# Kernel tuning notes

Hardware: AMD Instinct MI355X
Metric: run time of the kernel (lower is better)

## Reference

```python
import jax, jax.numpy as jnp
import numpy as np

C, H_HEADS, L_LEV, M_PTS = 256, 4, 3, 4
TAU0 = 1.0


def _ln(x, g, b, eps=1e-5):
    mu = x.mean(-1, keepdims=True)
    var = ((x - mu) ** 2).mean(-1, keepdims=True)
    return (x - mu) * jax.lax.rsqrt(var + eps) * g + b


def _grid_sample(v, grid):
    """Bilinear grid_sample, padding_mode='zeros', align_corners=True.
    v: [B,C,Hin,Win], grid: [B,N,2] (x,y) in [-1,1] -> [B,N,C]"""
    B, Cc, Hin, Win = v.shape
    x = (grid[..., 0] + 1.0) * 0.5 * (Win - 1)
    y = (grid[..., 1] + 1.0) * 0.5 * (Hin - 1)
    x0 = jnp.floor(x); y0 = jnp.floor(y)
    wx1 = x - x0; wy1 = y - y0
    x0i = x0.astype(jnp.int32); y0i = y0.astype(jnp.int32)
    vflat = v.reshape(B, Cc, Hin * Win).transpose(0, 2, 1)  # [B,HW,C]

    def tap(yi, xi, w):
        valid = ((xi >= 0) & (xi < Win) & (yi >= 0) & (yi < Hin)).astype(v.dtype)
        idx = jnp.clip(yi, 0, Hin - 1) * Win + jnp.clip(xi, 0, Win - 1)  # [B,N]
        g = jax.vmap(lambda vf, i: vf[i])(vflat, idx)  # [B,N,C]
        return g * (w * valid)[..., None]

    return (tap(y0i, x0i, (1 - wy1) * (1 - wx1))
            + tap(y0i, x0i + 1, (1 - wy1) * wx1)
            + tap(y0i + 1, x0i, wy1 * (1 - wx1))
            + tap(y0i + 1, x0i + 1, wy1 * wx1))


def setup_inputs() -> dict:
    key = jax.random.key(0)
    ks = jax.random.split(key, 32)
    B, Hq, Wq = 2, 64, 64
    cins = [256, 512, 1024]
    d = {
        'S':  jax.random.normal(ks[0], (B, C, Hq, Wq), jnp.float32),
        'f0': jax.random.normal(ks[1], (B, cins[0], 64, 64), jnp.float32),
        'f1': jax.random.normal(ks[2], (B, cins[1], 32, 32), jnp.float32),
        'f2': jax.random.normal(ks[3], (B, cins[2], 16, 16), jnp.float32),
        'sim': jax.random.uniform(ks[4], (B, 1, Hq, Wq), jnp.float32),
        # 1x1 conv value projections per level
        'vw0': jax.random.normal(ks[5], (C, cins[0]), jnp.float32) * 0.02,
        'vb0': jnp.zeros((C,), jnp.float32),
        'vw1': jax.random.normal(ks[6], (C, cins[1]), jnp.float32) * 0.02,
        'vb1': jnp.zeros((C,), jnp.float32),
        'vw2': jax.random.normal(ks[7], (C, cins[2]), jnp.float32) * 0.02,
        'vb2': jnp.zeros((C,), jnp.float32),
        'q_w': jax.random.normal(ks[8], (C, C), jnp.float32) * 0.02,
        'q_b': jnp.zeros((C,), jnp.float32),
        # offset/weight predictors (non-zero so sampling is nontrivial)
        'off_w': jax.random.normal(ks[9], (H_HEADS * L_LEV * M_PTS * 2, C), jnp.float32) * 0.01,
        'off_b': jnp.zeros((H_HEADS * L_LEV * M_PTS * 2,), jnp.float32),
        'wgt_w': jax.random.normal(ks[10], (H_HEADS * L_LEV * M_PTS, C), jnp.float32) * 0.02,
        'wgt_b': jnp.zeros((H_HEADS * L_LEV * M_PTS,), jnp.float32),
        'out_w': jax.random.normal(ks[11], (C, H_HEADS * C), jnp.float32) * 0.02,
        'out_b': jnp.zeros((C,), jnp.float32),
        'lnq_g': jnp.ones((C,), jnp.float32), 'lnq_b': jnp.zeros((C,), jnp.float32),
        'lno_g': jnp.ones((C,), jnp.float32), 'lno_b': jnp.zeros((C,), jnp.float32),
        'fc1_w': jax.random.normal(ks[12], (4 * C, C), jnp.float32) * 0.02,
        'fc1_b': jnp.zeros((4 * C,), jnp.float32),
        'fc2_w': jax.random.normal(ks[13], (C, 4 * C), jnp.float32) * 0.02,
        'fc2_b': jnp.zeros((C,), jnp.float32),
    }
    return d


def reference(S, f0, f1, f2, sim, vw0, vb0, vw1, vb1, vw2, vb2, q_w, q_b,
              off_w, off_b, wgt_w, wgt_b, out_w, out_b,
              lnq_g, lnq_b, lno_g, lno_b, fc1_w, fc1_b, fc2_w, fc2_b):
    B, Cc, Hq, Wq = S.shape
    Nq = Hq * Wq
    S_seq = S.reshape(B, Cc, Nq).transpose(0, 2, 1)  # [B,Nq,C]
    Q = _ln(S_seq @ q_w.T + q_b, lnq_g, lnq_b)

    # reference points in [0,1], (x,y)
    ys = jnp.linspace(0.5 / Hq, 1 - 0.5 / Hq, Hq)
    xs = jnp.linspace(0.5 / Wq, 1 - 0.5 / Wq, Wq)
    yy, xx = jnp.meshgrid(ys, xs, indexing='ij')
    ref = jnp.stack([xx, yy], axis=-1).reshape(1, Nq, 2)

    feats = [(f0, vw0, vb0), (f1, vw1, vb1), (f2, vw2, vb2)]
    V = [jnp.einsum('bchw,oc->bohw', f, w) + b[None, :, None, None] for f, w, b in feats]

    off = (Q @ off_w.T + off_b).reshape(B, Nq, H_HEADS, L_LEV, M_PTS, 2)
    wts = (Q @ wgt_w.T + wgt_b).reshape(B, Nq, H_HEADS, L_LEV, M_PTS)

    sim2 = sim[:, 0].reshape(B, Nq, 1)
    tau = TAU0 / (sim2 + 0.001)
    wts = wts / tau.reshape(B, Nq, 1, 1, 1)
    wts = jax.nn.softmax(wts.reshape(B, Nq, H_HEADS, L_LEV * M_PTS), axis=-1)
    wts = wts.reshape(B, Nq, H_HEADS, L_LEV, M_PTS)

    acc = jnp.zeros((B, Nq, H_HEADS, Cc), S.dtype)
    for l in range(L_LEV):
        g01 = ref.reshape(1, Nq, 1, 1, 2) + off[:, :, :, l]  # [B,Nq,H,M,2]
        g = jnp.clip(jnp.tanh(g01 * 2.0 - 1.0), -1.0, 1.0)
        samp = _grid_sample(V[l], g.reshape(B, Nq * H_HEADS * M_PTS, 2))
        samp = samp.reshape(B, Nq, H_HEADS, M_PTS, Cc)
        acc = acc + jnp.einsum('bqhmc,bqhm->bqhc', samp, wts[:, :, :, l])

    Y = acc.reshape(B, Nq, H_HEADS * Cc) @ out_w.T + out_b
    Z = _ln(S_seq + Y, lno_g, lno_b)
    h = jax.nn.gelu(Z @ fc1_w.T + fc1_b, approximate=False)
    Z = Z + (h @ fc2_w.T + fc2_b)
    return Z.transpose(0, 2, 1).reshape(B, Cc, Hq, Wq)
```

## Files before the change

kernel.cpp:

```cpp
#include <hip/hip_runtime.h>
#include <hip/hip_bf16.h>
#include <math.h>

#define NQ 4096
#define CC 256

typedef __attribute__((ext_vector_type(8))) short bfrag;
typedef __attribute__((ext_vector_type(4))) float ffrag;

__device__ inline unsigned short f2bf(float x) {
  __hip_bfloat16 h = __float2bfloat16(x);
  return *reinterpret_cast<unsigned short*>(&h);
}

__device__ inline float bf2f(unsigned short u) {
  return __uint_as_float(((unsigned)u) << 16);
}

__device__ inline void gload16(const void* g, void* l) {
  __builtin_amdgcn_global_load_lds(
      (const __attribute__((address_space(1))) void*)g,
      (__attribute__((address_space(3))) void*)l, 16, 0, 0);
}

__device__ void tr64(const float* __restrict__ src,
                     unsigned short* __restrict__ dstb, int Cin, int P,
                     int p0, int c0, int b, float (*t)[73]) {
  int tid = threadIdx.x;
  int rx = tid & 15, ry = tid >> 4;
  const float* Sb = src + (size_t)b * Cin * P + p0 + rx * 4;
  #pragma unroll
  for (int i = 0; i < 4; i++) {
    int r = ry + i * 16;
    float4 v = *(const float4*)(Sb + (size_t)(c0 + r) * P);
    t[r][rx * 4 + 0] = v.x; t[r][rx * 4 + 1] = v.y;
    t[r][rx * 4 + 2] = v.z; t[r][rx * 4 + 3] = v.w;
  }
  __syncthreads();
  size_t ob = (size_t)b * P * Cin;
  #pragma unroll
  for (int i = 0; i < 4; i++) {
    int pr = ry + i * 16;
    float x0 = t[rx * 4 + 0][pr], x1 = t[rx * 4 + 1][pr];
    float x2 = t[rx * 4 + 2][pr], x3 = t[rx * 4 + 3][pr];
    size_t idx = ob + (size_t)(p0 + pr) * Cin + c0 + rx * 4;
    ushort4 u4;
    u4.x = f2bf(x0); u4.y = f2bf(x1); u4.z = f2bf(x2); u4.w = f2bf(x3);
    *(ushort4*)(dstb + idx) = u4;
  }
}

__global__ __launch_bounds__(256)
void prep_all_k(const float* S, const float* f0, const float* f1, const float* f2,
                const float* q_w, const float* off_w, const float* wgt_w,
                const float* vw0, const float* vw1, const float* vw2,
                const float* out_w, const float* fc1_w, const float* fc2_w,
                const float* off_b, const float* wgt_b,
                unsigned short* Sbf,
                unsigned short* Xf0, unsigned short* Xf1, unsigned short* Xf2,
                unsigned short* q_wb, unsigned short* owb,
                unsigned short* vw0b, unsigned short* vw1b, unsigned short* vw2b,
                unsigned short* out_wb, unsigned short* fc1_wb,
                unsigned short* fc2_wb, float* bias144) {
  __shared__ float t[64][73];
  int bid = blockIdx.x;
  if (bid < 512) {
    int l = bid;
    tr64(S, Sbf, 256, 4096, (l & 63) * 64, ((l >> 6) & 3) * 64, l >> 8, t);
  } else if (bid < 1024) {
    int l = bid - 512;
    tr64(f0, Xf0, 256, 4096, (l & 63) * 64, ((l >> 6) & 3) * 64, l >> 8, t);
  } else if (bid < 1280) {
    int l = bid - 1024;
    tr64(f1, Xf1, 512, 1024, (l & 15) * 64, ((l >> 4) & 7) * 64, l >> 7, t);
  } else if (bid < 1408) {
    int l = bid - 1280;
    tr64(f2, Xf2, 1024, 256, (l & 3) * 64, ((l >> 2) & 15) * 64, l >> 6, t);
  } else if (bid < 2688) {
    int i4 = (bid - 1408) * 256 + threadIdx.x;
    const float* src; unsigned short* dst;
    if (i4 < 16384)       { src = q_w;   dst = q_wb; }
    else if (i4 < 32768)  { i4 -= 16384;  src = vw0;   dst = vw0b; }
    else if (i4 < 65536)  { i4 -= 32768;  src = vw1;   dst = vw1b; }
    else if (i4 < 131072) { i4 -= 65536;  src = vw2;   dst = vw2b; }
    else if (i4 < 196608) { i4 -= 131072; src = out_w; dst = out_wb; }
    else if (i4 < 262144) { i4 -= 196608; src = fc1_w; dst = fc1_wb; }
    else                  { i4 -= 262144; src = fc2_w; dst = fc2_wb; }
    float4 v = ((const float4*)src)[i4];
    ushort4 u; u.x = f2bf(v.x); u.y = f2bf(v.y); u.z = f2bf(v.z); u.w = f2bf(v.w);
    ((ushort4*)dst)[i4] = u;
  } else {
    int e = (bid - 2688) * 256 + threadIdx.x;
    float v = (e < 24576) ? off_w[e] : (e < 36864 ? wgt_w[e - 24576] : 0.f);
    owb[e] = f2bf(v);
    if (e < 96) bias144[e] = off_b[e];
    else if (e < 144) bias144[e] = wgt_b[e - 96];
  }
}

template<int BM, int BN, int WM, int WN, int EPI>
__device__ __forceinline__ void gemm_body(
    const unsigned short* __restrict__ A, const unsigned short* __restrict__ B,
    const float* __restrict__ bias, float* __restrict__ outf,
    unsigned short* __restrict__ outb, int N, int Kloop, int lda, int ldb,
    int ldo, const unsigned short* __restrict__ Zres, float* __restrict__ outT,
    int m0, int n0, unsigned short* As, unsigned short* Bs) {
  constexpr int MI = BM / (WM * 16), NI = BN / (WN * 16);
  constexpr int TA = BM / 8, TB = BN / 8;
  constexpr int LBM = (BM == 32) ? 5 : (BM == 64) ? 6 : 7;
  constexpr int LBN = (BN == 64) ? 6 : (BN == 128) ? 7 : 8;
  int tid = threadIdx.x, wave = tid >> 6, lane = tid & 63;
  int quad = lane >> 4, l16 = lane & 15;
  int wm = wave / WN, wn = wave % WN;
  const int mbase = wm * (BM / WM), nbase = wn * (BN / WN);

  ffrag acc[MI][NI];
  #pragma unroll
  for (int i = 0; i < MI; i++)
    #pragma unroll
    for (int j = 0; j < NI; j++) acc[i][j] = (ffrag)0.f;

  for (int k0 = 0; k0 < Kloop; k0 += 64) {
    __syncthreads();
    for (int t = wave; t < TA + TB; t += 4) {
      if (t < TA) {
        int s = t * 64 + lane;
        int kc = s >> LBM, r = s & (BM - 1);
        gload16(A + (size_t)(m0 + r) * lda + k0 + kc * 8, (char*)As + t * 1024);
      } else {
        int s = (t - TA) * 64 + lane;
        int kc = s >> LBN, r = s & (BN - 1);
        gload16(B + (size_t)(n0 + r) * ldb + k0 + kc * 8, (char*)Bs + (t - TA) * 1024);
      }
    }
    __syncthreads();
    #pragma unroll
    for (int ks = 0; ks < 2; ks++) {
      bfrag af[MI], bf[NI];
      #pragma unroll
      for (int mi = 0; mi < MI; mi++)
        af[mi] = *(const bfrag*)(As + ((((ks * 4 + quad) << LBM) + mbase + mi * 16 + l16) << 3));
      #pragma unroll
      for (int ni = 0; ni < NI; ni++)
        bf[ni] = *(const bfrag*)(Bs + ((((ks * 4 + quad) << LBN) + nbase + ni * 16 + l16) << 3));
      #pragma unroll
      for (int mi = 0; mi < MI; mi++)
        #pragma unroll
        for (int ni = 0; ni < NI; ni++)
          acc[mi][ni] = __builtin_amdgcn_mfma_f32_16x16x32_bf16(
              af[mi], bf[ni], acc[mi][ni], 0, 0, 0);
    }
  }

  if (EPI == 2) {
    #pragma unroll
    for (int mi = 0; mi < MI; mi++) {
      int mrow = m0 + mbase + mi * 16 + quad * 4;
      int bb = mrow >> 12, q0 = mrow & (NQ - 1);
      #pragma unroll
      for (int ni = 0; ni < NI; ni++) {
        int n = n0 + nbase + ni * 16 + l16;
        float bv = bias[n];
        float4 v;
        v.x = acc[mi][ni][0] + bv + bf2f(Zres[(size_t)(mrow + 0) * CC + n]);
        v.y = acc[mi][ni][1] + bv + bf2f(Zres[(size_t)(mrow + 1) * CC + n]);
        v.z = acc[mi][ni][2] + bv + bf2f(Zres[(size_t)(mrow + 2) * CC + n]);
        v.w = acc[mi][ni][3] + bv + bf2f(Zres[(size_t)(mrow + 3) * CC + n]);
        *(float4*)(outT + ((size_t)(bb * CC + n)) * NQ + q0) = v;
      }
    }
  } else {
    #pragma unroll
    for (int mi = 0; mi < MI; mi++) {
      int mrow = m0 + mbase + mi * 16 + quad * 4;
      #pragma unroll
      for (int ni = 0; ni < NI; ni++) {
        int n = n0 + nbase + ni * 16 + l16;
        if (n < N) {
          float bv = (EPI == 4) ? 0.f : bias[n];
          #pragma unroll
          for (int r = 0; r < 4; r++) {
            float v = acc[mi][ni][r] + bv;
            if (EPI == 1) {
              v = 0.5f * v * (1.f + erff(v * 0.70710678118654752f));
              outb[(size_t)(mrow + r) * ldo + n] = f2bf(v);
            } else if (EPI == 3) {
              outb[(size_t)(mrow + r) * ldo + n] = f2bf(v);
            } else {
              outf[(size_t)(mrow + r) * ldo + n] = v;
            }
          }
        }
      }
    }
  }
}

__device__ __forceinline__ void gemm_ln_q(
    const unsigned short* __restrict__ A, const unsigned short* __restrict__ B,
    const float* __restrict__ bias, unsigned short* __restrict__ outb,
    const float* __restrict__ g, const float* __restrict__ be,
    int m0, char* sm) {
  unsigned short* As = (unsigned short*)sm;
  unsigned short* Bs = (unsigned short*)(sm + 4096);
  float* L = (float*)sm;
  const int K = 256;

  int tid = threadIdx.x, wave = tid >> 6, lane = tid & 63;
  int quad = lane >> 4, l16 = lane & 15;

  ffrag acc[2][4];
  #pragma unroll
  for (int i = 0; i < 2; i++)
    #pragma unroll
    for (int j = 0; j < 4; j++) acc[i][j] = (ffrag)0.f;

  for (int k0 = 0; k0 < K; k0 += 64) {
    __syncthreads();
    for (int t = wave; t < 36; t += 4) {
      if (t < 4) {
        int s = t * 64 + lane;
        int kc = s >> 5, r = s & 31;
        gload16(A + (size_t)(m0 + r) * K + k0 + kc * 8, sm + t * 1024);
      } else {
        int s = (t - 4) * 64 + lane;
        int kc = s >> 8, r = s & 255;
        gload16(B + (size_t)r * K + k0 + kc * 8, sm + 4096 + (t - 4) * 1024);
      }
    }
    __syncthreads();
    #pragma unroll
    for (int ks = 0; ks < 2; ks++) {
      bfrag af[2], bf[4];
      #pragma unroll
      for (int mi = 0; mi < 2; mi++)
        af[mi] = *(const bfrag*)(As + ((((ks * 4 + quad) << 5) + mi * 16 + l16) << 3));
      #pragma unroll
      for (int ni = 0; ni < 4; ni++)
        bf[ni] = *(const bfrag*)(Bs + ((((ks * 4 + quad) << 8) + wave * 64 + ni * 16 + l16) << 3));
      #pragma unroll
      for (int mi = 0; mi < 2; mi++)
        #pragma unroll
        for (int ni = 0; ni < 4; ni++)
          acc[mi][ni] = __builtin_amdgcn_mfma_f32_16x16x32_bf16(
              af[mi], bf[ni], acc[mi][ni], 0, 0, 0);
    }
  }
  __syncthreads();

  #pragma unroll
  for (int mi = 0; mi < 2; mi++) {
    int row = mi * 16 + quad * 4;
    #pragma unroll
    for (int ni = 0; ni < 4; ni++) {
      int col = wave * 64 + ni * 16 + l16;
      float bv = bias[col];
      #pragma unroll
      for (int r = 0; r < 4; r++)
        L[(row + r) * 264 + col] = acc[mi][ni][r] + bv;
    }
  }
  __syncthreads();

  int row = tid >> 3, j = tid & 7;
  int seg = ((j + row) & 7) * 32;
  const float* Lr = L + row * 264 + seg;
  float s1 = 0.f, s2 = 0.f;
  #pragma unroll
  for (int i = 0; i < 8; i++) {
    float4 t4 = *(const float4*)(Lr + i * 4);
    s1 += t4.x + t4.y + t4.z + t4.w;
    s2 += t4.x * t4.x + t4.y * t4.y + t4.z * t4.z + t4.w * t4.w;
  }
  #pragma unroll
  for (int o = 1; o < 8; o <<= 1) {
    s1 += __shfl_xor(s1, o);
    s2 += __shfl_xor(s2, o);
  }
  float mu = s1 * (1.f / 256.f);
  float var = s2 * (1.f / 256.f) - mu * mu;
  float rs = rsqrtf(var + 1e-5f);
  int gm = m0 + row;
  #pragma unroll
  for (int i = 0; i < 8; i++) {
    int col = seg + i * 4;
    float4 t4 = *(const float4*)(Lr + i * 4);
    float4 gg = *(const float4*)(g + col);
    float4 bb4 = *(const float4*)(be + col);
    ushort4 ub;
    ub.x = f2bf((t4.x - mu) * rs * gg.x + bb4.x);
    ub.y = f2bf((t4.y - mu) * rs * gg.y + bb4.y);
    ub.z = f2bf((t4.z - mu) * rs * gg.z + bb4.z);
    ub.w = f2bf((t4.w - mu) * rs * gg.w + bb4.w);
    *(ushort4*)(outb + (size_t)gm * CC + col) = ub;
  }
}

__global__ __launch_bounds__(256)
void qv_k(const unsigned short* Sbf, const unsigned short* q_wb, const float* q_b,
          const float* lnq_g, const float* lnq_b, unsigned short* Qbf,
          const unsigned short* Xf0, const unsigned short* Xf1,
          const unsigned short* Xf2, const unsigned short* vw0b,
          const unsigned short* vw1b, const unsigned short* vw2b,
          const float* vb0, unsigned short* V0b, float* Vp1, float* Vp2) {
  __shared__ __attribute__((aligned(16))) char sm[36864];
  int bid = blockIdx.x;
  unsigned short* As = (unsigned short*)sm;
  unsigned short* Bs = (unsigned short*)(sm + 8192);
  if (bid < 256) {
    gemm_ln_q(Sbf, q_wb, q_b, Qbf, lnq_g, lnq_b, bid * 32, sm);
  } else if (bid < 512) {
    int t = bid - 256;
    gemm_body<64, 128, 2, 2, 3>(Xf0, vw0b, vb0, nullptr, V0b, 256, 256, 256, 256,
                                256, nullptr, nullptr, (t >> 1) * 64, (t & 1) * 128, As, Bs);
  } else if (bid < 640) {
    int l = bid - 512, ks = l >> 6, t = l & 63;
    gemm_body<64, 128, 2, 2, 4>(Xf1 + ks * 256, vw1b + ks * 256, nullptr,
                                Vp1 + (size_t)ks * 524288, nullptr, 256, 256, 512, 512,
                                256, nullptr, nullptr, (t >> 1) * 64, (t & 1) * 128, As, Bs);
  } else {
    int l = bid - 640, ks = l >> 4, t = l & 15;
    gemm_body<64, 128, 2, 2, 4>(Xf2 + ks * 256, vw2b + ks * 256, nullptr,
                                Vp2 + (size_t)ks * 131072, nullptr, 256, 256, 1024, 1024,
                                256, nullptr, nullptr, (t >> 1) * 64, (t & 1) * 128, As, Bs);
  }
}

__global__ __launch_bounds__(256)
void offv_k(const unsigned short* Qbf, const unsigned short* owb,
            const float* bias144, float* offwgt,
            const float* Vp1, const float* Vp2, const float* vb1,
            const float* vb2, unsigned short* V1b, unsigned short* V2b) {
  __shared__ __attribute__((aligned(16))) unsigned short As[4096];
  __shared__ __attribute__((aligned(16))) unsigned short Bs[16384];
  int bid = blockIdx.x;
  if (bid < 128) {
    gemm_body<64, 256, 2, 2, 0>(Qbf, owb, bias144, offwgt, nullptr, 144, 256, 256,
                                256, 144, nullptr, nullptr, bid * 64, 0, As, Bs);
  } else if (bid < 640) {
    int e4 = (bid - 128) * 256 + threadIdx.x;
    const float4* P = (const float4*)Vp1;
    float4 a = P[e4], b = P[e4 + 131072];
    float4 bb = *(const float4*)(vb1 + ((e4 << 2) & 255));
    ushort4 u;
    u.x = f2bf(a.x + b.x + bb.x); u.y = f2bf(a.y + b.y + bb.y);
    u.z = f2bf(a.z + b.z + bb.z); u.w = f2bf(a.w + b.w + bb.w);
    ((ushort4*)V1b)[e4] = u;
  } else {
    int e4 = (bid - 640) * 256 + threadIdx.x;
    const float4* P = (const float4*)Vp2;
    float4 a = P[e4], b = P[e4 + 32768], c = P[e4 + 65536], d = P[e4 + 98304];
    float4 bb = *(const float4*)(vb2 + ((e4 << 2) & 255));
    ushort4 u;
    u.x = f2bf(a.x + b.x + c.x + d.x + bb.x);
    u.y = f2bf(a.y + b.y + c.y + d.y + bb.y);
    u.z = f2bf(a.z + b.z + c.z + d.z + bb.z);
    u.w = f2bf(a.w + b.w + c.w + d.w + bb.w);
    ((ushort4*)V2b)[e4] = u;
  }
}

__global__ __launch_bounds__(256)
void outA_k(const unsigned short* accbf, const unsigned short* out_wb, float* Op) {
  __shared__ __attribute__((aligned(16))) char sm[36864];
  int ks = blockIdx.y;
  gemm_body<32, 256, 1, 4, 4>(accbf + ks * 512, out_wb + ks * 512, nullptr,
                              Op + (size_t)ks * 2097152, nullptr, 256, 512, 1024,
                              1024, 256, nullptr, nullptr, blockIdx.x * 32, 0,
                              (unsigned short*)sm, (unsigned short*)(sm + 4096));
}

__global__ __launch_bounds__(256)
void outB_k(const float* __restrict__ Op, const float* __restrict__ S,
            const float* __restrict__ out_b, const float* __restrict__ g,
            const float* __restrict__ be, unsigned short* __restrict__ Zbf) {
  __shared__ float Ls[16][264];
  int q0 = blockIdx.x * 16;
  int b = q0 >> 12, qq = q0 & (NQ - 1);
  int t = threadIdx.x;
  {
    int cs = t >> 2, j = (t & 3) * 4;
    #pragma unroll
    for (int c0 = 0; c0 < 256; c0 += 64) {
      float4 sv = *(const float4*)(S + (((size_t)(b * 256 + c0 + cs)) << 12) + qq + j);
      Ls[j + 0][c0 + cs] = sv.x; Ls[j + 1][c0 + cs] = sv.y;
      Ls[j + 2][c0 + cs] = sv.z; Ls[j + 3][c0 + cs] = sv.w;
    }
  }
  __syncthreads();
  int c = t;
  float bv = out_b[c];
  float val[16];
  #pragma unroll
  for (int r = 0; r < 16; r++) {
    size_t idx = (size_t)(q0 + r) * 256 + c;
    val[r] = Op[idx] + Op[idx + 2097152] + bv + Ls[r][c];
  }
  __syncthreads();
  #pragma unroll
  for (int r = 0; r < 16; r++) Ls[r][c] = val[r];
  __syncthreads();
  int row = t >> 4, lg = t & 15;
  const float* Lr = &Ls[row][lg * 16];
  float s1 = 0.f, s2 = 0.f;
  #pragma unroll
  for (int i = 0; i < 4; i++) {
    float4 t4 = *(const float4*)(Lr + i * 4);
    s1 += t4.x + t4.y + t4.z + t4.w;
    s2 += t4.x * t4.x + t4.y * t4.y + t4.z * t4.z + t4.w * t4.w;
  }
  #pragma unroll
  for (int o = 1; o < 16; o <<= 1) {
    s1 += __shfl_xor(s1, o);
    s2 += __shfl_xor(s2, o);
  }
  float mu = s1 * (1.f / 256.f);
  float var = s2 * (1.f / 256.f) - mu * mu;
  float rs = rsqrtf(var + 1e-5f);
  int gm = q0 + row;
  #pragma unroll
  for (int i = 0; i < 4; i++) {
    int col = lg * 16 + i * 4;
    float4 t4 = *(const float4*)(Lr + i * 4);
    float4 gg = *(const float4*)(g + col);
    float4 bb4 = *(const float4*)(be + col);
    ushort4 ub;
    ub.x = f2bf((t4.x - mu) * rs * gg.x + bb4.x);
    ub.y = f2bf((t4.y - mu) * rs * gg.y + bb4.y);
    ub.z = f2bf((t4.z - mu) * rs * gg.z + bb4.z);
    ub.w = f2bf((t4.w - mu) * rs * gg.w + bb4.w);
    *(ushort4*)(Zbf + (size_t)gm * CC + col) = ub;
  }
}

__global__ __launch_bounds__(256)
void fc1_k(const unsigned short* Zbf, const unsigned short* fc1_wb,
           const float* fc1_b, unsigned short* hbf) {
  __shared__ __attribute__((aligned(16))) unsigned short As[4096];
  __shared__ __attribute__((aligned(16))) unsigned short Bs[16384];
  gemm_body<64, 256, 2, 2, 1>(Zbf, fc1_wb, fc1_b, nullptr, hbf, 1024, 256, 256,
                              256, 1024, nullptr, nullptr,
                              blockIdx.y * 64, blockIdx.x * 256, As, Bs);
}

__global__ __launch_bounds__(256)
void fc2_k(const unsigned short* hbf, const unsigned short* fc2_wb,
           const float* fc2_b, const unsigned short* Zbf, float* outp) {
  __shared__ __attribute__((aligned(16))) unsigned short As[4096];
  __shared__ __attribute__((aligned(16))) unsigned short Bs[4096];
  gemm_body<64, 64, 2, 2, 2>(hbf, fc2_wb, fc2_b, nullptr, nullptr, 256, 1024,
                             1024, 1024, 256, Zbf, outp,
                             blockIdx.y * 64, blockIdx.x * 64, As, Bs);
}

__global__ __launch_bounds__(256)
void sample_k(const float* __restrict__ ow, const float* __restrict__ sim,
              const unsigned short* __restrict__ V0, const unsigned short* __restrict__ V1,
              const unsigned short* __restrict__ V2, unsigned short* __restrict__ acc) {
  int bn = blockIdx.x;
  int q = ((bn & 7) << 10) | (bn >> 3);
  int b = q >> 12, n = q & (NQ - 1);
  int tid = threadIdx.x, head = tid >> 6, lane = tid & 63;
  int half = lane >> 5, l32 = lane & 31;

  __shared__ float s_w[48];
  __shared__ int   s_xy[48][2];
  __shared__ float s_f[48][2];
  __shared__ uint2 s_ow[192];

  if (tid < 48) {
    int hh = tid / 12, pt = tid % 12, l = pt >> 2, mm = pt & 3;
    int oidx = (hh * 3 + l) * 4 + mm;
    float offx = ow[(size_t)q * 144 + oidx * 2 + 0];
    float offy = ow[(size_t)q * 144 + oidx * 2 + 1];
    float refx = ((n & 63) + 0.5f) * (1.f / 64.f);
    float refy = ((n >> 6) + 0.5f) * (1.f / 64.f);
    float gx = tanhf((refx + offx) * 2.f - 1.f);
    float gy = tanhf((refy + offy) * 2.f - 1.f);
    gx = fminf(1.f, fmaxf(-1.f, gx));
    gy = fminf(1.f, fmaxf(-1.f, gy));
    int Wl = 64 >> l;
    float x = (gx + 1.f) * 0.5f * (float)(Wl - 1);
    float y = (gy + 1.f) * 0.5f * (float)(Wl - 1);
    float x0 = floorf(x), y0 = floorf(y);
    s_xy[tid][0] = (int)x0;
    s_xy[tid][1] = (int)y0;
    s_f[tid][0] = x - x0;
    s_f[tid][1] = y - y0;
    s_w[tid] = ow[(size_t)q * 144 + 96 + oidx] * (sim[q] + 0.001f);
  }
  __syncthreads();
  if (tid < 4) {
    float mx = -1e30f;
    #pragma unroll
    for (int i = 0; i < 12; i++) mx = fmaxf(mx, s_w[tid * 12 + i]);
    float e[12], ssum = 0.f;
    #pragma unroll
    for (int i = 0; i < 12; i++) { e[i] = expf(s_w[tid * 12 + i] - mx); ssum += e[i]; }
    float inv = 1.f / ssum;
    #pragma unroll
    for (int i = 0; i < 12; i++) s_w[tid * 12 + i] = e[i] * inv;
  }
  __syncthreads();
  if (tid < 192) {
    int s = tid >> 2, tap = tid & 3;
    int l = (s % 12) >> 2;
    int Wl = 64 >> l;
    int X = s_xy[s][0] + (tap & 1), Y = s_xy[s][1] + (tap >> 1);
    bool valid = (X >= 0 && X < Wl && Y >= 0 && Y < Wl);
    float wx = (tap & 1) ? s_f[s][0] : 1.f - s_f[s][0];
    float wy = (tap >> 1) ? s_f[s][1] : 1.f - s_f[s][1];
    float twt = valid ? s_w[s] * wx * wy : 0.f;
    int Xc = min(max(X, 0), Wl - 1), Yc = min(max(Y, 0), Wl - 1);
    s_ow[tid].x = (unsigned)((Yc * Wl + Xc) << 8);
    s_ow[tid].y = __float_as_uint(twt);
  }
  __syncthreads();

  const unsigned short* B0 = V0 + (size_t)b * 4096 * CC;
  const unsigned short* B1 = V1 + (size_t)b * 1024 * CC;
  const unsigned short* B2 = V2 + (size_t)b * 256 * CC;
  int ch8 = l32 * 8;
  float a0 = 0.f, a1 = 0.f, a2 = 0.f, a3 = 0.f;
  float a4 = 0.f, a5 = 0.f, a6 = 0.f, a7 = 0.f;
  #pragma unroll
  for (int it = 0; it < 24; it++) {
    const unsigned short* base = (it < 8) ? B0 : (it < 16) ? B1 : B2;
    uint2 owv = s_ow[head * 48 + it * 2 + half];
    float w = __uint_as_float(owv.y);
    const uint4 u = *(const uint4*)(base + owv.x + ch8);
    a0 = fmaf(w, __uint_as_float(u.x << 16), a0);
    a1 = fmaf(w, __uint_as_float(u.x & 0xffff0000u), a1);
    a2 = fmaf(w, __uint_as_float(u.y << 16), a2);
    a3 = fmaf(w, __uint_as_float(u.y & 0xffff0000u), a3);
    a4 = fmaf(w, __uint_as_float(u.z << 16), a4);
    a5 = fmaf(w, __uint_as_float(u.z & 0xffff0000u), a5);
    a6 = fmaf(w, __uint_as_float(u.w << 16), a6);
    a7 = fmaf(w, __uint_as_float(u.w & 0xffff0000u), a7);
  }
  a0 += __shfl_xor(a0, 32); a1 += __shfl_xor(a1, 32);
  a2 += __shfl_xor(a2, 32); a3 += __shfl_xor(a3, 32);
  a4 += __shfl_xor(a4, 32); a5 += __shfl_xor(a5, 32);
  a6 += __shfl_xor(a6, 32); a7 += __shfl_xor(a7, 32);
  if (half == 0) {
    uint4 r;
    r.x = (unsigned)f2bf(a0) | ((unsigned)f2bf(a1) << 16);
    r.y = (unsigned)f2bf(a2) | ((unsigned)f2bf(a3) << 16);
    r.z = (unsigned)f2bf(a4) | ((unsigned)f2bf(a5) << 16);
    r.w = (unsigned)f2bf(a6) | ((unsigned)f2bf(a7) << 16);
    *(uint4*)(acc + (size_t)q * 1024 + head * CC + ch8) = r;
  }
}

extern "C" void kernel_launch(void* const* d_in, const int* in_sizes, int n_in,
                              void* d_out, int out_size, void* d_ws, size_t ws_size,
                              hipStream_t stream) {
  const float* S     = (const float*)d_in[0];
  const float* f0    = (const float*)d_in[1];
  const float* f1    = (const float*)d_in[2];
  const float* f2    = (const float*)d_in[3];
  const float* sim   = (const float*)d_in[4];
  const float* vw0   = (const float*)d_in[5];
  const float* vb0   = (const float*)d_in[6];
  const float* vw1   = (const float*)d_in[7];
  const float* vb1   = (const float*)d_in[8];
  const float* vw2   = (const float*)d_in[9];
  const float* vb2   = (const float*)d_in[10];
  const float* q_w   = (const float*)d_in[11];
  const float* q_b   = (const float*)d_in[12];
  const float* off_w = (const float*)d_in[13];
  const float* off_b = (const float*)d_in[14];
  const float* wgt_w = (const float*)d_in[15];
  const float* wgt_b = (const float*)d_in[16];
  const float* out_w = (const float*)d_in[17];
  const float* out_b = (const float*)d_in[18];
  const float* lnq_g = (const float*)d_in[19];
  const float* lnq_b = (const float*)d_in[20];
  const float* lno_g = (const float*)d_in[21];
  const float* lno_b = (const float*)d_in[22];
  const float* fc1_w = (const float*)d_in[23];
  const float* fc1_b = (const float*)d_in[24];
  const float* fc2_w = (const float*)d_in[25];
  const float* fc2_b = (const float*)d_in[26];

  char* p = (char*)d_ws;
  float* offwgt = (float*)p; p += 4718592;
  float* bias144 = (float*)p; p += 1024;
  float* Pp     = (float*)p; p += 16777216;
  float* Vp1    = (float*)p; p += 4194304;
  float* Vp2    = (float*)p; p += 2097152;
  unsigned short* Sbf   = (unsigned short*)p; p += 4194304;
  unsigned short* Qbf   = (unsigned short*)p; p += 4194304;
  unsigned short* accbf = (unsigned short*)p; p += 16777216;
  unsigned short* V0b   = (unsigned short*)p; p += 4194304;
  unsigned short* V1b   = (unsigned short*)p; p += 1048576;
  unsigned short* V2b   = (unsigned short*)p; p += 262144;
  unsigned short* q_wb   = (unsigned short*)p; p += 131072;
  unsigned short* owb    = (unsigned short*)p; p += 131072;
  unsigned short* vw0b   = (unsigned short*)p; p += 131072;
  unsigned short* vw1b   = (unsigned short*)p; p += 262144;
  unsigned short* vw2b   = (unsigned short*)p; p += 524288;
  unsigned short* out_wb = (unsigned short*)p; p += 524288;
  unsigned short* fc1_wb = (unsigned short*)p; p += 524288;
  unsigned short* fc2_wb = (unsigned short*)p; p += 524288;

  unsigned short* Xf0 = accbf;
  unsigned short* Xf1 = accbf + 2097152;
  unsigned short* Xf2 = accbf + 3145728;
  unsigned short* Zbf = Qbf;
  unsigned short* hbf = accbf;
  float* outp = (float*)d_out;

  prep_all_k<<<2944, 256, 0, stream>>>(S, f0, f1, f2, q_w, off_w, wgt_w,
      vw0, vw1, vw2, out_w, fc1_w, fc2_w, off_b, wgt_b,
      Sbf, Xf0, Xf1, Xf2, q_wb, owb, vw0b, vw1b, vw2b, out_wb,
      fc1_wb, fc2_wb, bias144);

  qv_k<<<704, 256, 0, stream>>>(Sbf, q_wb, q_b, lnq_g, lnq_b, Qbf,
      Xf0, Xf1, Xf2, vw0b, vw1b, vw2b, vb0, V0b, Vp1, Vp2);

  offv_k<<<768, 256, 0, stream>>>(Qbf, owb, bias144, offwgt,
      Vp1, Vp2, vb1, vb2, V1b, V2b);

  sample_k<<<8192, 256, 0, stream>>>(offwgt, sim, V0b, V1b, V2b, accbf);

  outA_k<<<dim3(256, 2), 256, 0, stream>>>(accbf, out_wb, Pp);

  outB_k<<<512, 256, 0, stream>>>(Pp, S, out_b, lno_g, lno_b, Zbf);

  fc1_k<<<dim3(4, 128), 256, 0, stream>>>(Zbf, fc1_wb, fc1_b, hbf);

  fc2_k<<<dim3(4, 128), 256, 0, stream>>>(hbf, fc2_wb, fc2_b, Zbf, outp);
}
```

Measured before the change: 263.8 us.

## Fuse all stages into one persistent kernel with software grid barriers

Replaces the eight separate kernel launches with a single persistent kernel of 768 blocks. Each stage runs its original work items in a grid-stride loop, and stages are separated by atomic-counter grid barriers whose counters are zeroed by a memset before launch. The goal is to remove launch overhead and inter-kernel gaps. In exchange it adds barrier spin costs and fixed-grid load imbalance, and correctness depends on all 768 blocks being co-resident, which launch_bounds(256,3) is meant to allow.

New measurement: 959.9 us. 3.64x slower.

```diff
diff --git a/kernel.cpp b/kernel.cpp
--- a/kernel.cpp
+++ b/kernel.cpp
@@ -4,6 +4,7 @@
 
 #define NQ 4096
 #define CC 256
+#define GRID 768
 
 typedef __attribute__((ext_vector_type(8))) short bfrag;
 typedef __attribute__((ext_vector_type(4))) float ffrag;
@@ -23,79 +24,28 @@
       (__attribute__((address_space(3))) void*)l, 16, 0, 0);
 }
 
-__device__ void tr64(const float* __restrict__ src,
-                     unsigned short* __restrict__ dstb, int Cin, int P,
-                     int p0, int c0, int b, float (*t)[73]) {
-  int tid = threadIdx.x;
-  int rx = tid & 15, ry = tid >> 4;
-  const float* Sb = src + (size_t)b * Cin * P + p0 + rx * 4;
-  #pragma unroll
-  for (int i = 0; i < 4; i++) {
-    int r = ry + i * 16;
-    float4 v = *(const float4*)(Sb + (size_t)(c0 + r) * P);
-    t[r][rx * 4 + 0] = v.x; t[r][rx * 4 + 1] = v.y;
-    t[r][rx * 4 + 2] = v.z; t[r][rx * 4 + 3] = v.w;
-  }
-  __syncthreads();
-  size_t ob = (size_t)b * P * Cin;
-  #pragma unroll
-  for (int i = 0; i < 4; i++) {
-    int pr = ry + i * 16;
-    float x0 = t[rx * 4 + 0][pr], x1 = t[rx * 4 + 1][pr];
-    float x2 = t[rx * 4 + 2][pr], x3 = t[rx * 4 + 3][pr];
-    size_t idx = ob + (size_t)(p0 + pr) * Cin + c0 + rx * 4;
-    ushort4 u4;
-    u4.x = f2bf(x0); u4.y = f2bf(x1); u4.z = f2bf(x2); u4.w = f2bf(x3);
-    *(ushort4*)(dstb + idx) = u4;
-  }
-}
-
-__global__ __launch_bounds__(256)
-void prep_all_k(const float* S, const float* f0, const float* f1, const float* f2,
-                const float* q_w, const float* off_w, const float* wgt_w,
-                const float* vw0, const float* vw1, const float* vw2,
-                const float* out_w, const float* fc1_w, const float* fc2_w,
-                const float* off_b, const float* wgt_b,
-                unsigned short* Sbf,
-                unsigned short* Xf0, unsigned short* Xf1, unsigned short* Xf2,
-                unsigned short* q_wb, unsigned short* owb,
-                unsigned short* vw0b, unsigned short* vw1b, unsigned short* vw2b,
-                unsigned short* out_wb, unsigned short* fc1_wb,
-                unsigned short* fc2_wb, float* bias144) {
-  __shared__ float t[64][73];
-  int bid = blockIdx.x;
-  if (bid < 512) {
-    int l = bid;
-    tr64(S, Sbf, 256, 4096, (l & 63) * 64, ((l >> 6) & 3) * 64, l >> 8, t);
-  } else if (bid < 1024) {
-    int l = bid - 512;
-    tr64(f0, Xf0, 256, 4096, (l & 63) * 64, ((l >> 6) & 3) * 64, l >> 8, t);
-  } else if (bid < 1280) {
-    int l = bid - 1024;
-    tr64(f1, Xf1, 512, 1024, (l & 15) * 64, ((l >> 4) & 7) * 64, l >> 7, t);
-  } else if (bid < 1408) {
-    int l = bid - 1280;
-    tr64(f2, Xf2, 1024, 256, (l & 3) * 64, ((l >> 2) & 15) * 64, l >> 6, t);
-  } else if (bid < 2688) {
-    int i4 = (bid - 1408) * 256 + threadIdx.x;
-    const float* src; unsigned short* dst;
-    if (i4 < 16384)       { src = q_w;   dst = q_wb; }
-    else if (i4 < 32768)  { i4 -= 16384;  src = vw0;   dst = vw0b; }
-    else if (i4 < 65536)  { i4 -= 32768;  src = vw1;   dst = vw1b; }
-    else if (i4 < 131072) { i4 -= 65536;  src = vw2;   dst = vw2b; }
-    else if (i4 < 196608) { i4 -= 131072; src = out_w; dst = out_wb; }
-    else if (i4 < 262144) { i4 -= 196608; src = fc1_w; dst = fc1_wb; }
-    else                  { i4 -= 262144; src = fc2_w; dst = fc2_wb; }
-    float4 v = ((const float4*)src)[i4];
-    ushort4 u; u.x = f2bf(v.x); u.y = f2bf(v.y); u.z = f2bf(v.z); u.w = f2bf(v.w);
-    ((ushort4*)dst)[i4] = u;
-  } else {
-    int e = (bid - 2688) * 256 + threadIdx.x;
-    float v = (e < 24576) ? off_w[e] : (e < 36864 ? wgt_w[e - 24576] : 0.f);
-    owb[e] = f2bf(v);
-    if (e < 96) bias144[e] = off_b[e];
-    else if (e < 144) bias144[e] = wgt_b[e - 96];
-  }
+struct MP {
+  const float *S, *f0, *f1, *f2, *sim;
+  const float *vw0, *vb0, *vw1, *vb1, *vw2, *vb2;
+  const float *q_w, *q_b, *off_w, *off_b, *wgt_w, *wgt_b, *out_w, *out_b;
+  const float *lnq_g, *lnq_b, *lno_g, *lno_b;
+  const float *fc1_w, *fc1_b, *fc2_w, *fc2_b;
+  float *offwgt, *bias144, *Pp, *Vp1, *Vp2, *outp;
+  unsigned short *Sbf, *Qbf, *accbf, *V0b, *V1b, *V2b;
+  unsigned short *q_wb, *owb, *vw0b, *vw1b, *vw2b, *out_wb, *fc1_wb, *fc2_wb;
+  unsigned *bars;
+};
+
+__device__ inline void gbar(unsigned* bars, int i) {
+  __syncthreads();
+  if (threadIdx.x == 0) {
+    unsigned* slot = bars + i * 16;
+    __threadfence();
+    atomicAdd(slot, 1u);
+    while (atomicAdd(slot, 0u) < GRID) __builtin_amdgcn_s_sleep(8);
+    __threadfence();
+  }
+  __syncthreads();
 }
 
 template<int BM, int BN, int WM, int WN, int EPI>
@@ -196,7 +146,71 @@
   }
 }
 
-__device__ __forceinline__ void gemm_ln_q(
+__device__ void tr64(const float* __restrict__ src,
+                     unsigned short* __restrict__ dstb, int Cin, int P,
+                     int p0, int c0, int b, float (*t)[73]) {
+  int tid = threadIdx.x;
+  int rx = tid & 15, ry = tid >> 4;
+  const float* Sb = src + (size_t)b * Cin * P + p0 + rx * 4;
+  #pragma unroll
+  for (int i = 0; i < 4; i++) {
+    int r = ry + i * 16;
+    float4 v = *(const float4*)(Sb + (size_t)(c0 + r) * P);
+    t[r][rx * 4 + 0] = v.x; t[r][rx * 4 + 1] = v.y;
+    t[r][rx * 4 + 2] = v.z; t[r][rx * 4 + 3] = v.w;
+  }
+  __syncthreads();
+  size_t ob = (size_t)b * P * Cin;
+  #pragma unroll
+  for (int i = 0; i < 4; i++) {
+    int pr = ry + i * 16;
+    float x0 = t[rx * 4 + 0][pr], x1 = t[rx * 4 + 1][pr];
+    float x2 = t[rx * 4 + 2][pr], x3 = t[rx * 4 + 3][pr];
+    size_t idx = ob + (size_t)(p0 + pr) * Cin + c0 + rx * 4;
+    ushort4 u4;
+    u4.x = f2bf(x0); u4.y = f2bf(x1); u4.z = f2bf(x2); u4.w = f2bf(x3);
+    *(ushort4*)(dstb + idx) = u4;
+  }
+}
+
+static __device__ void prep_item(const MP& p, int bid, char* sm) {
+  __syncthreads();
+  float (*t)[73] = (float(*)[73])sm;
+  if (bid < 512) {
+    int l = bid;
+    tr64(p.S, p.Sbf, 256, 4096, (l & 63) * 64, ((l >> 6) & 3) * 64, l >> 8, t);
+  } else if (bid < 1024) {
+    int l = bid - 512;
+    tr64(p.f0, p.accbf, 256, 4096, (l & 63) * 64, ((l >> 6) & 3) * 64, l >> 8, t);
+  } else if (bid < 1280) {
+    int l = bid - 1024;
+    tr64(p.f1, p.accbf + 2097152, 512, 1024, (l & 15) * 64, ((l >> 4) & 7) * 64, l >> 7, t);
+  } else if (bid < 1408) {
+    int l = bid - 1280;
+    tr64(p.f2, p.accbf + 3145728, 1024, 256, (l & 3) * 64, ((l >> 2) & 15) * 64, l >> 6, t);
+  } else if (bid < 2688) {
+    int i4 = (bid - 1408) * 256 + threadIdx.x;
+    const float* src; unsigned short* dst;
+    if (i4 < 16384)       { src = p.q_w;   dst = p.q_wb; }
+    else if (i4 < 32768)  { i4 -= 16384;  src = p.vw0;   dst = p.vw0b; }
+    else if (i4 < 65536)  { i4 -= 32768;  src = p.vw1;   dst = p.vw1b; }
+    else if (i4 < 131072) { i4 -= 65536;  src = p.vw2;   dst = p.vw2b; }
+    else if (i4 < 196608) { i4 -= 131072; src = p.out_w; dst = p.out_wb; }
+    else if (i4 < 262144) { i4 -= 196608; src = p.fc1_w; dst = p.fc1_wb; }
+    else                  { i4 -= 262144; src = p.fc2_w; dst = p.fc2_wb; }
+    float4 v = ((const float4*)src)[i4];
+    ushort4 u; u.x = f2bf(v.x); u.y = f2bf(v.y); u.z = f2bf(v.z); u.w = f2bf(v.w);
+    ((ushort4*)dst)[i4] = u;
+  } else {
+    int e = (bid - 2688) * 256 + threadIdx.x;
+    float v = (e < 24576) ? p.off_w[e] : (e < 36864 ? p.wgt_w[e - 24576] : 0.f);
+    p.owb[e] = f2bf(v);
+    if (e < 96) p.bias144[e] = p.off_b[e];
+    else if (e < 144) p.bias144[e] = p.wgt_b[e - 96];
+  }
+}
+
+static __device__ void gemm_ln_q(
     const unsigned short* __restrict__ A, const unsigned short* __restrict__ B,
     const float* __restrict__ bias, unsigned short* __restrict__ outb,
     const float* __restrict__ g, const float* __restrict__ be,
@@ -296,183 +310,83 @@
   }
 }
 
-__global__ __launch_bounds__(256)
-void qv_k(const unsigned short* Sbf, const unsigned short* q_wb, const float* q_b,
-          const float* lnq_g, const float* lnq_b, unsigned short* Qbf,
-          const unsigned short* Xf0, const unsigned short* Xf1,
-          const unsigned short* Xf2, const unsigned short* vw0b,
-          const unsigned short* vw1b, const unsigned short* vw2b,
-          const float* vb0, unsigned short* V0b, float* Vp1, float* Vp2) {
-  __shared__ __attribute__((aligned(16))) char sm[36864];
-  int bid = blockIdx.x;
+static __device__ void qv_item(const MP& p, int bid, char* sm) {
   unsigned short* As = (unsigned short*)sm;
   unsigned short* Bs = (unsigned short*)(sm + 8192);
+  const unsigned short* Xf0 = p.accbf;
+  const unsigned short* Xf1 = p.accbf + 2097152;
+  const unsigned short* Xf2 = p.accbf + 3145728;
   if (bid < 256) {
-    gemm_ln_q(Sbf, q_wb, q_b, Qbf, lnq_g, lnq_b, bid * 32, sm);
+    gemm_ln_q(p.Sbf, p.q_wb, p.q_b, p.Qbf, p.lnq_g, p.lnq_b, bid * 32, sm);
   } else if (bid < 512) {
     int t = bid - 256;
-    gemm_body<64, 128, 2, 2, 3>(Xf0, vw0b, vb0, nullptr, V0b, 256, 256, 256, 256,
-                                256, nullptr, nullptr, (t >> 1) * 64, (t & 1) * 128, As, Bs);
+    gemm_body<64, 128, 2, 2, 3>(Xf0, p.vw0b, p.vb0, nullptr, p.V0b, 256, 256,
+                                256, 256, 256, nullptr, nullptr,
+                                (t >> 1) * 64, (t & 1) * 128, As, Bs);
   } else if (bid < 640) {
     int l = bid - 512, ks = l >> 6, t = l & 63;
-    gemm_body<64, 128, 2, 2, 4>(Xf1 + ks * 256, vw1b + ks * 256, nullptr,
-                                Vp1 + (size_t)ks * 524288, nullptr, 256, 256, 512, 512,
-                                256, nullptr, nullptr, (t >> 1) * 64, (t & 1) * 128, As, Bs);
+    gemm_body<64, 128, 2, 2, 4>(Xf1 + ks * 256, p.vw1b + ks * 256, nullptr,
+                                p.Vp1 + (size_t)ks * 524288, nullptr, 256, 256,
+                                512, 512, 256, nullptr, nullptr,
+                                (t >> 1) * 64, (t & 1) * 128, As, Bs);
   } else {
     int l = bid - 640, ks = l >> 4, t = l & 15;
-    gemm_body<64, 128, 2, 2, 4>(Xf2 + ks * 256, vw2b + ks * 256, nullptr,
-                                Vp2 + (size_t)ks * 131072, nullptr, 256, 256, 1024, 1024,
-                                256, nullptr, nullptr, (t >> 1) * 64, (t & 1) * 128, As, Bs);
-  }
-}
-
-__global__ __launch_bounds__(256)
-void offv_k(const unsigned short* Qbf, const unsigned short* owb,
-            const float* bias144, float* offwgt,
-            const float* Vp1, const float* Vp2, const float* vb1,
-            const float* vb2, unsigned short* V1b, unsigned short* V2b) {
-  __shared__ __attribute__((aligned(16))) unsigned short As[4096];
-  __shared__ __attribute__((aligned(16))) unsigned short Bs[16384];
-  int bid = blockIdx.x;
+    gemm_body<64, 128, 2, 2, 4>(Xf2 + ks * 256, p.vw2b + ks * 256, nullptr,
+                                p.Vp2 + (size_t)ks * 131072, nullptr, 256, 256,
+                                1024, 1024, 256, nullptr, nullptr,
+                                (t >> 1) * 64, (t & 1) * 128, As, Bs);
+  }
+}
+
+static __device__ void offv_item(const MP& p, int bid, char* sm) {
   if (bid < 128) {
-    gemm_body<64, 256, 2, 2, 0>(Qbf, owb, bias144, offwgt, nullptr, 144, 256, 256,
-                                256, 144, nullptr, nullptr, bid * 64, 0, As, Bs);
+    unsigned short* As = (unsigned short*)sm;
+    unsigned short* Bs = (unsigned short*)(sm + 8192);
+    gemm_body<64, 256, 2, 2, 0>(p.Qbf, p.owb, p.bias144, p.offwgt, nullptr, 144,
+                                256, 256, 256, 144, nullptr, nullptr,
+                                bid * 64, 0, As, Bs);
   } else if (bid < 640) {
     int e4 = (bid - 128) * 256 + threadIdx.x;
-    const float4* P = (const float4*)Vp1;
-    float4 a = P[e4], b = P[e4 + 131072];
-    float4 bb = *(const float4*)(vb1 + ((e4 << 2) & 255));
+    const float4* P4 = (const float4*)p.Vp1;
+    float4 a = P4[e4], b = P4[e4 + 131072];
+    float4 bb = *(const float4*)(p.vb1 + ((e4 << 2) & 255));
     ushort4 u;
     u.x = f2bf(a.x + b.x + bb.x); u.y = f2bf(a.y + b.y + bb.y);
     u.z = f2bf(a.z + b.z + bb.z); u.w = f2bf(a.w + b.w + bb.w);
-    ((ushort4*)V1b)[e4] = u;
+    ((ushort4*)p.V1b)[e4] = u;
   } else {
     int e4 = (bid - 640) * 256 + threadIdx.x;
-    const float4* P = (const float4*)Vp2;
-    float4 a = P[e4], b = P[e4 + 32768], c = P[e4 + 65536], d = P[e4 + 98304];
-    float4 bb = *(const float4*)(vb2 + ((e4 << 2) & 255));
+    const float4* P4 = (const float4*)p.Vp2;
+    float4 a = P4[e4], b = P4[e4 + 32768], c = P4[e4 + 65536], d = P4[e4 + 98304];
+    float4 bb = *(const float4*)(p.vb2 + ((e4 << 2) & 255));
     ushort4 u;
     u.x = f2bf(a.x + b.x + c.x + d.x + bb.x);
     u.y = f2bf(a.y + b.y + c.y + d.y + bb.y);
     u.z = f2bf(a.z + b.z + c.z + d.z + bb.z);
     u.w = f2bf(a.w + b.w + c.w + d.w + bb.w);
-    ((ushort4*)V2b)[e4] = u;
-  }
-}
-
-__global__ __launch_bounds__(256)
-void outA_k(const unsigned short* accbf, const unsigned short* out_wb, float* Op) {
-  __shared__ __attribute__((aligned(16))) char sm[36864];
-  int ks = blockIdx.y;
-  gemm_body<32, 256, 1, 4, 4>(accbf + ks * 512, out_wb + ks * 512, nullptr,
-                              Op + (size_t)ks * 2097152, nullptr, 256, 512, 1024,
-                              1024, 256, nullptr, nullptr, blockIdx.x * 32, 0,
-                              (unsigned short*)sm, (unsigned short*)(sm + 4096));
-}
-
-__global__ __launch_bounds__(256)
-void outB_k(const float* __restrict__ Op, const float* __restrict__ S,
-            const float* __restrict__ out_b, const float* __restrict__ g,
-            const float* __restrict__ be, unsigned short* __restrict__ Zbf) {
-  __shared__ float Ls[16][264];
-  int q0 = blockIdx.x * 16;
-  int b = q0 >> 12, qq = q0 & (NQ - 1);
-  int t = threadIdx.x;
-  {
-    int cs = t >> 2, j = (t & 3) * 4;
-    #pragma unroll
-    for (int c0 = 0; c0 < 256; c0 += 64) {
-      float4 sv = *(const float4*)(S + (((size_t)(b * 256 + c0 + cs)) << 12) + qq + j);
-      Ls[j + 0][c0 + cs] = sv.x; Ls[j + 1][c0 + cs] = sv.y;
-      Ls[j + 2][c0 + cs] = sv.z; Ls[j + 3][c0 + cs] = sv.w;
-    }
-  }
-  __syncthreads();
-  int c = t;
-  float bv = out_b[c];
-  float val[16];
-  #pragma unroll
-  for (int r = 0; r < 16; r++) {
-    size_t idx = (size_t)(q0 + r) * 256 + c;
-    val[r] = Op[idx] + Op[idx + 2097152] + bv + Ls[r][c];
-  }
-  __syncthreads();
-  #pragma unroll
-  for (int r = 0; r < 16; r++) Ls[r][c] = val[r];
-  __syncthreads();
-  int row = t >> 4, lg = t & 15;
-  const float* Lr = &Ls[row][lg * 16];
-  float s1 = 0.f, s2 = 0.f;
-  #pragma unroll
-  for (int i = 0; i < 4; i++) {
-    float4 t4 = *(const float4*)(Lr + i * 4);
-    s1 += t4.x + t4.y + t4.z + t4.w;
-    s2 += t4.x * t4.x + t4.y * t4.y + t4.z * t4.z + t4.w * t4.w;
-  }
-  #pragma unroll
-  for (int o = 1; o < 16; o <<= 1) {
-    s1 += __shfl_xor(s1, o);
-    s2 += __shfl_xor(s2, o);
-  }
-  float mu = s1 * (1.f / 256.f);
-  float var = s2 * (1.f / 256.f) - mu * mu;
-  float rs = rsqrtf(var + 1e-5f);
-  int gm = q0 + row;
-  #pragma unroll
-  for (int i = 0; i < 4; i++) {
-    int col = lg * 16 + i * 4;
-    float4 t4 = *(const float4*)(Lr + i * 4);
-    float4 gg = *(const float4*)(g + col);
-    float4 bb4 = *(const float4*)(be + col);
-    ushort4 ub;
-    ub.x = f2bf((t4.x - mu) * rs * gg.x + bb4.x);
-    ub.y = f2bf((t4.y - mu) * rs * gg.y + bb4.y);
-    ub.z = f2bf((t4.z - mu) * rs * gg.z + bb4.z);
-    ub.w = f2bf((t4.w - mu) * rs * gg.w + bb4.w);
-    *(ushort4*)(Zbf + (size_t)gm * CC + col) = ub;
-  }
-}
-
-__global__ __launch_bounds__(256)
-void fc1_k(const unsigned short* Zbf, const unsigned short* fc1_wb,
-           const float* fc1_b, unsigned short* hbf) {
-  __shared__ __attribute__((aligned(16))) unsigned short As[4096];
-  __shared__ __attribute__((aligned(16))) unsigned short Bs[16384];
-  gemm_body<64, 256, 2, 2, 1>(Zbf, fc1_wb, fc1_b, nullptr, hbf, 1024, 256, 256,
-                              256, 1024, nullptr, nullptr,
-                              blockIdx.y * 64, blockIdx.x * 256, As, Bs);
-}
-
-__global__ __launch_bounds__(256)
-void fc2_k(const unsigned short* hbf, const unsigned short* fc2_wb,
-           const float* fc2_b, const unsigned short* Zbf, float* outp) {
-  __shared__ __attribute__((aligned(16))) unsigned short As[4096];
-  __shared__ __attribute__((aligned(16))) unsigned short Bs[4096];
-  gemm_body<64, 64, 2, 2, 2>(hbf, fc2_wb, fc2_b, nullptr, nullptr, 256, 1024,
-                             1024, 1024, 256, Zbf, outp,
-                             blockIdx.y * 64, blockIdx.x * 64, As, Bs);
-}
-
-__global__ __launch_bounds__(256)
-void sample_k(const float* __restrict__ ow, const float* __restrict__ sim,
-              const unsigned short* __restrict__ V0, const unsigned short* __restrict__ V1,
-              const unsigned short* __restrict__ V2, unsigned short* __restrict__ acc) {
-  int bn = blockIdx.x;
+    ((ushort4*)p.V2b)[e4] = u;
+  }
+}
+
+static __device__ void sample_item(const MP& p, int bn, char* smraw) {
+  struct SSh {
+    float w[48];
+    int xy[48][2];
+    float f[48][2];
+    uint2 ow2[192];
+  };
+  SSh& sh = *(SSh*)smraw;
   int q = ((bn & 7) << 10) | (bn >> 3);
   int b = q >> 12, n = q & (NQ - 1);
   int tid = threadIdx.x, head = tid >> 6, lane = tid & 63;
   int half = lane >> 5, l32 = lane & 31;
 
-  __shared__ float s_w[48];
-  __shared__ int   s_xy[48][2];
-  __shared__ float s_f[48][2];
-  __shared__ uint2 s_ow[192];
-
+  __syncthreads();
   if (tid < 48) {
     int hh = tid / 12, pt = tid % 12, l = pt >> 2, mm = pt & 3;
     int oidx = (hh * 3 + l) * 4 + mm;
-    float offx = ow[(size_t)q * 144 + oidx * 2 + 0];
-    float offy = ow[(size_t)q * 144 + oidx * 2 + 1];
+    float offx = p.offwgt[(size_t)q * 144 + oidx * 2 + 0];
+    float offy = p.offwgt[(size_t)q * 144 + oidx * 2 + 1];
     float refx = ((n & 63) + 0.5f) * (1.f / 64.f);
     float refy = ((n >> 6) + 0.5f) * (1.f / 64.f);
     float gx = tanhf((refx + offx) * 2.f - 1.f);
@@ -483,50 +397,50 @@
     float x = (gx + 1.f) * 0.5f * (float)(Wl - 1);
     float y = (gy + 1.f) * 0.5f * (float)(Wl - 1);
     float x0 = floorf(x), y0 = floorf(y);
-    s_xy[tid][0] = (int)x0;
-    s_xy[tid][1] = (int)y0;
-    s_f[tid][0] = x - x0;
-    s_f[tid][1] = y - y0;
-    s_w[tid] = ow[(size_t)q * 144 + 96 + oidx] * (sim[q] + 0.001f);
+    sh.xy[tid][0] = (int)x0;
+    sh.xy[tid][1] = (int)y0;
+    sh.f[tid][0] = x - x0;
+    sh.f[tid][1] = y - y0;
+    sh.w[tid] = p.offwgt[(size_t)q * 144 + 96 + oidx] * (p.sim[q] + 0.001f);
   }
   __syncthreads();
   if (tid < 4) {
     float mx = -1e30f;
     #pragma unroll
-    for (int i = 0; i < 12; i++) mx = fmaxf(mx, s_w[tid * 12 + i]);
+    for (int i = 0; i < 12; i++) mx = fmaxf(mx, sh.w[tid * 12 + i]);
     float e[12], ssum = 0.f;
     #pragma unroll
-    for (int i = 0; i < 12; i++) { e[i] = expf(s_w[tid * 12 + i] - mx); ssum += e[i]; }
+    for (int i = 0; i < 12; i++) { e[i] = expf(sh.w[tid * 12 + i] - mx); ssum += e[i]; }
     float inv = 1.f / ssum;
     #pragma unroll
-    for (int i = 0; i < 12; i++) s_w[tid * 12 + i] = e[i] * inv;
+    for (int i = 0; i < 12; i++) sh.w[tid * 12 + i] = e[i] * inv;
   }
   __syncthreads();
   if (tid < 192) {
     int s = tid >> 2, tap = tid & 3;
     int l = (s % 12) >> 2;
     int Wl = 64 >> l;
-    int X = s_xy[s][0] + (tap & 1), Y = s_xy[s][1] + (tap >> 1);
+    int X = sh.xy[s][0] + (tap & 1), Y = sh.xy[s][1] + (tap >> 1);
     bool valid = (X >= 0 && X < Wl && Y >= 0 && Y < Wl);
-    float wx = (tap & 1) ? s_f[s][0] : 1.f - s_f[s][0];
-    float wy = (tap >> 1) ? s_f[s][1] : 1.f - s_f[s][1];
-    float twt = valid ? s_w[s] * wx * wy : 0.f;
+    float wx = (tap & 1) ? sh.f[s][0] : 1.f - sh.f[s][0];
+    float wy = (tap >> 1) ? sh.f[s][1] : 1.f - sh.f[s][1];
+    float twt = valid ? sh.w[s] * wx * wy : 0.f;
     int Xc = min(max(X, 0), Wl - 1), Yc = min(max(Y, 0), Wl - 1);
-    s_ow[tid].x = (unsigned)((Yc * Wl + Xc) << 8);
-    s_ow[tid].y = __float_as_uint(twt);
-  }
-  __syncthreads();
-
-  const unsigned short* B0 = V0 + (size_t)b * 4096 * CC;
-  const unsigned short* B1 = V1 + (size_t)b * 1024 * CC;
-  const unsigned short* B2 = V2 + (size_t)b * 256 * CC;
+    sh.ow2[tid].x = (unsigned)((Yc * Wl + Xc) << 8);
+    sh.ow2[tid].y = __float_as_uint(twt);
+  }
+  __syncthreads();
+
+  const unsigned short* B0 = p.V0b + (size_t)b * 4096 * CC;
+  const unsigned short* B1 = p.V1b + (size_t)b * 1024 * CC;
+  const unsigned short* B2 = p.V2b + (size_t)b * 256 * CC;
   int ch8 = l32 * 8;
   float a0 = 0.f, a1 = 0.f, a2 = 0.f, a3 = 0.f;
   float a4 = 0.f, a5 = 0.f, a6 = 0.f, a7 = 0.f;
   #pragma unroll
   for (int it = 0; it < 24; it++) {
     const unsigned short* base = (it < 8) ? B0 : (it < 16) ? B1 : B2;
-    uint2 owv = s_ow[head * 48 + it * 2 + half];
+    uint2 owv = sh.ow2[head * 48 + it * 2 + half];
     float w = __uint_as_float(owv.y);
     const uint4 u = *(const uint4*)(base + owv.x + ch8);
     a0 = fmaf(w, __uint_as_float(u.x << 16), a0);
@@ -548,87 +462,178 @@
     r.y = (unsigned)f2bf(a2) | ((unsigned)f2bf(a3) << 16);
     r.z = (unsigned)f2bf(a4) | ((unsigned)f2bf(a5) << 16);
     r.w = (unsigned)f2bf(a6) | ((unsigned)f2bf(a7) << 16);
-    *(uint4*)(acc + (size_t)q * 1024 + head * CC + ch8) = r;
-  }
+    *(uint4*)(p.accbf + (size_t)q * 1024 + head * CC + ch8) = r;
+  }
+}
+
+static __device__ void outA_item(const MP& p, int bid, char* sm) {
+  int ks = bid >> 8, m = bid & 255;
+  gemm_body<32, 256, 1, 4, 4>(p.accbf + ks * 512, p.out_wb + ks * 512, nullptr,
+                              p.Pp + (size_t)ks * 2097152, nullptr, 256, 512,
+                              1024, 1024, 256, nullptr, nullptr, m * 32, 0,
+                              (unsigned short*)sm, (unsigned short*)(sm + 4096));
+}
+
+static __device__ void outB_item(const MP& p, int bid, char* smraw) {
+  float (*Ls)[264] = (float(*)[264])smraw;
+  int q0 = bid * 16;
+  int b = q0 >> 12, qq = q0 & (NQ - 1);
+  int t = threadIdx.x;
+  {
+    int cs = t >> 2, j = (t & 3) * 4;
+    #pragma unroll
+    for (int c0 = 0; c0 < 256; c0 += 64) {
+      float4 sv = *(const float4*)(p.S + (((size_t)(b * 256 + c0 + cs)) << 12) + qq + j);
+      Ls[j + 0][c0 + cs] = sv.x; Ls[j + 1][c0 + cs] = sv.y;
+      Ls[j + 2][c0 + cs] = sv.z; Ls[j + 3][c0 + cs] = sv.w;
+    }
+  }
+  __syncthreads();
+  int c = t;
+  float bv = p.out_b[c];
+  float val[16];
+  #pragma unroll
+  for (int r = 0; r < 16; r++) {
+    size_t idx = (size_t)(q0 + r) * 256 + c;
+    val[r] = p.Pp[idx] + p.Pp[idx + 2097152] + bv + Ls[r][c];
+  }
+  __syncthreads();
+  #pragma unroll
+  for (int r = 0; r < 16; r++) Ls[r][c] = val[r];
+  __syncthreads();
+  int row = t >> 4, lg = t & 15;
+  const float* Lr = &Ls[row][lg * 16];
+  float s1 = 0.f, s2 = 0.f;
+  #pragma unroll
+  for (int i = 0; i < 4; i++) {
+    float4 t4 = *(const float4*)(Lr + i * 4);
+    s1 += t4.x + t4.y + t4.z + t4.w;
+    s2 += t4.x * t4.x + t4.y * t4.y + t4.z * t4.z + t4.w * t4.w;
+  }
+  #pragma unroll
+  for (int o = 1; o < 16; o <<= 1) {
+    s1 += __shfl_xor(s1, o);
+    s2 += __shfl_xor(s2, o);
+  }
+  float mu = s1 * (1.f / 256.f);
+  float var = s2 * (1.f / 256.f) - mu * mu;
+  float rs = rsqrtf(var + 1e-5f);
+  int gm = q0 + row;
+  #pragma unroll
+  for (int i = 0; i < 4; i++) {
+    int col = lg * 16 + i * 4;
+    float4 t4 = *(const float4*)(Lr + i * 4);
+    float4 gg = *(const float4*)(p.lno_g + col);
+    float4 bb4 = *(const float4*)(p.lno_b + col);
+    ushort4 ub;
+    ub.x = f2bf((t4.x - mu) * rs * gg.x + bb4.x);
+    ub.y = f2bf((t4.y - mu) * rs * gg.y + bb4.y);
+    ub.z = f2bf((t4.z - mu) * rs * gg.z + bb4.z);
+    ub.w = f2bf((t4.w - mu) * rs * gg.w + bb4.w);
+    *(ushort4*)(p.Qbf + (size_t)gm * CC + col) = ub;
+  }
+}
+
+static __device__ void fc1_item(const MP& p, int bid, char* sm) {
+  int nx = bid & 3, my = bid >> 2;
+  gemm_body<64, 256, 2, 2, 1>(p.Qbf, p.fc1_wb, p.fc1_b, nullptr, p.accbf, 1024,
+                              256, 256, 256, 1024, nullptr, nullptr,
+                              my * 64, nx * 256,
+                              (unsigned short*)sm, (unsigned short*)(sm + 8192));
+}
+
+static __device__ void fc2_item(const MP& p, int bid, char* sm) {
+  int nx = bid & 3, my = bid >> 2;
+  gemm_body<64, 64, 2, 2, 2>(p.accbf, p.fc2_wb, p.fc2_b, nullptr, nullptr, 256,
+                             1024, 1024, 1024, 256, p.Qbf, p.outp,
+                             my * 64, nx * 64,
+                             (unsigned short*)sm, (unsigned short*)(sm + 8192));
+}
+
+__global__ __launch_bounds__(256, 3)
+void mega_k(MP p) {
+  __shared__ __attribute__((aligned(16))) char sm[40960];
+  int bid = blockIdx.x;
+
+  for (int w = bid; w < 2944; w += GRID) prep_item(p, w, sm);
+  gbar(p.bars, 0);
+
+  if (bid < 704) qv_item(p, bid, sm);
+  gbar(p.bars, 1);
+
+  offv_item(p, bid, sm);
+  gbar(p.bars, 2);
+
+  for (int w = bid; w < 8192; w += GRID) sample_item(p, w, sm);
+  gbar(p.bars, 3);
+
+  if (bid < 512) outA_item(p, bid, sm);
+  gbar(p.bars, 4);
+
+  if (bid < 512) outB_item(p, bid, sm);
+  gbar(p.bars, 5);
+
+  if (bid < 512) fc1_item(p, bid, sm);
+  gbar(p.bars, 6);
+
+  if (bid < 512) fc2_item(p, bid, sm);
 }
 
 extern "C" void kernel_launch(void* const* d_in, const int* in_sizes, int n_in,
                               void* d_out, int out_size, void* d_ws, size_t ws_size,
                               hipStream_t stream) {
-  const float* S     = (const float*)d_in[0];
-  const float* f0    = (const float*)d_in[1];
-  const float* f1    = (const float*)d_in[2];
-  const float* f2    = (const float*)d_in[3];
-  const float* sim   = (const float*)d_in[4];
-  const float* vw0   = (const float*)d_in[5];
-  const float* vb0   = (const float*)d_in[6];
-  const float* vw1   = (const float*)d_in[7];
-  const float* vb1   = (const float*)d_in[8];
-  const float* vw2   = (const float*)d_in[9];
-  const float* vb2   = (const float*)d_in[10];
-  const float* q_w   = (const float*)d_in[11];
-  const float* q_b   = (const float*)d_in[12];
-  const float* off_w = (const float*)d_in[13];
-  const float* off_b = (const float*)d_in[14];
-  const float* wgt_w = (const float*)d_in[15];
-  const float* wgt_b = (const float*)d_in[16];
-  const float* out_w = (const float*)d_in[17];
-  const float* out_b = (const float*)d_in[18];
-  const float* lnq_g = (const float*)d_in[19];
-  const float* lnq_b = (const float*)d_in[20];
-  const float* lno_g = (const float*)d_in[21];
-  const float* lno_b = (const float*)d_in[22];
-  const float* fc1_w = (const float*)d_in[23];
-  const float* fc1_b = (const float*)d_in[24];
-  const float* fc2_w = (const float*)d_in[25];
-  const float* fc2_b = (const float*)d_in[26];
-
-  char* p = (char*)d_ws;
-  float* offwgt = (float*)p; p += 4718592;
-  float* bias144 = (float*)p; p += 1024;
-  float* Pp     = (float*)p; p += 16777216;
-  float* Vp1    = (float*)p; p += 4194304;
-  float* Vp2    = (float*)p; p += 2097152;
-  unsigned short* Sbf   = (unsigned short*)p; p += 4194304;
-  unsigned short* Qbf   = (unsigned short*)p; p += 4194304;
-  unsigned short* accbf = (unsigned short*)p; p += 16777216;
-  unsigned short* V0b   = (unsigned short*)p; p += 4194304;
-  unsigned short* V1b   = (unsigned short*)p; p += 1048576;
-  unsigned short* V2b   = (unsigned short*)p; p += 262144;
-  unsigned short* q_wb   = (unsigned short*)p; p += 131072;
-  unsigned short* owb    = (unsigned short*)p; p += 131072;
-  unsigned short* vw0b   = (unsigned short*)p; p += 131072;
-  unsigned short* vw1b   = (unsigned short*)p; p += 262144;
-  unsigned short* vw2b   = (unsigned short*)p; p += 524288;
-  unsigned short* out_wb = (unsigned short*)p; p += 524288;
-  unsigned short* fc1_wb = (unsigned short*)p; p += 524288;
-  unsigned short* fc2_wb = (unsigned short*)p; p += 524288;
-
-  unsigned short* Xf0 = accbf;
-  unsigned short* Xf1 = accbf + 2097152;
-  unsigned short* Xf2 = accbf + 3145728;
-  unsigned short* Zbf = Qbf;
-  unsigned short* hbf = accbf;
-  float* outp = (float*)d_out;
-
-  prep_all_k<<<2944, 256, 0, stream>>>(S, f0, f1, f2, q_w, off_w, wgt_w,
-      vw0, vw1, vw2, out_w, fc1_w, fc2_w, off_b, wgt_b,
-      Sbf, Xf0, Xf1, Xf2, q_wb, owb, vw0b, vw1b, vw2b, out_wb,
-      fc1_wb, fc2_wb, bias144);
-
-  qv_k<<<704, 256, 0, stream>>>(Sbf, q_wb, q_b, lnq_g, lnq_b, Qbf,
-      Xf0, Xf1, Xf2, vw0b, vw1b, vw2b, vb0, V0b, Vp1, Vp2);
-
-  offv_k<<<768, 256, 0, stream>>>(Qbf, owb, bias144, offwgt,
-      Vp1, Vp2, vb1, vb2, V1b, V2b);
-
-  sample_k<<<8192, 256, 0, stream>>>(offwgt, sim, V0b, V1b, V2b, accbf);
-
-  outA_k<<<dim3(256, 2), 256, 0, stream>>>(accbf, out_wb, Pp);
-
-  outB_k<<<512, 256, 0, stream>>>(Pp, S, out_b, lno_g, lno_b, Zbf);
-
-  fc1_k<<<dim3(4, 128), 256, 0, stream>>>(Zbf, fc1_wb, fc1_b, hbf);
-
-  fc2_k<<<dim3(4, 128), 256, 0, stream>>>(hbf, fc2_wb, fc2_b, Zbf, outp);
-}
+  MP p;
+  p.S     = (const float*)d_in[0];
+  p.f0    = (const float*)d_in[1];
+  p.f1    = (const float*)d_in[2];
+  p.f2    = (const float*)d_in[3];
+  p.sim   = (const float*)d_in[4];
+  p.vw0   = (const float*)d_in[5];
+  p.vb0   = (const float*)d_in[6];
+  p.vw1   = (const float*)d_in[7];
+  p.vb1   = (const float*)d_in[8];
+  p.vw2   = (const float*)d_in[9];
+  p.vb2   = (const float*)d_in[10];
+  p.q_w   = (const float*)d_in[11];
+  p.q_b   = (const float*)d_in[12];
+  p.off_w = (const float*)d_in[13];
+  p.off_b = (const float*)d_in[14];
+  p.wgt_w = (const float*)d_in[15];
+  p.wgt_b = (const float*)d_in[16];
+  p.out_w = (const float*)d_in[17];
+  p.out_b = (const float*)d_in[18];
+  p.lnq_g = (const float*)d_in[19];
+  p.lnq_b = (const float*)d_in[20];
+  p.lno_g = (const float*)d_in[21];
+  p.lno_b = (const float*)d_in[22];
+  p.fc1_w = (const float*)d_in[23];
+  p.fc1_b = (const float*)d_in[24];
+  p.fc2_w = (const float*)d_in[25];
+  p.fc2_b = (const float*)d_in[26];
+
+  char* w = (char*)d_ws;
+  p.bars    = (unsigned*)w; w += 1024;
+  p.offwgt  = (float*)w; w += 4718592;
+  p.bias144 = (float*)w; w += 1024;
+  p.Pp      = (float*)w; w += 16777216;
+  p.Vp1     = (float*)w; w += 4194304;
+  p.Vp2     = (float*)w; w += 2097152;
+  p.Sbf     = (unsigned short*)w; w += 4194304;
+  p.Qbf     = (unsigned short*)w; w += 4194304;
+  p.accbf   = (unsigned short*)w; w += 16777216;
+  p.V0b     = (unsigned short*)w; w += 4194304;
+  p.V1b     = (unsigned short*)w; w += 1048576;
+  p.V2b     = (unsigned short*)w; w += 262144;
+  p.q_wb    = (unsigned short*)w; w += 131072;
+  p.owb     = (unsigned short*)w; w += 131072;
+  p.vw0b    = (unsigned short*)w; w += 131072;
+  p.vw1b    = (unsigned short*)w; w += 262144;
+  p.vw2b    = (unsigned short*)w; w += 524288;
+  p.out_wb  = (unsigned short*)w; w += 524288;
+  p.fc1_wb  = (unsigned short*)w; w += 524288;
+  p.fc2_wb  = (unsigned short*)w; w += 524288;
+  p.outp    = (float*)d_out;
+
+  hipMemsetAsync(p.bars, 0, 1024, stream);
+  mega_k<<<GRID, 256, 0, stream>>>(p);
+}
```
